# Kernel optimization log

Measured on AMD Instinct MI355X. Metric: run time of the kernel, lower is better.

Reference implementation:

```python
import jax, jax.numpy as jnp
import numpy as np

NUM_USERS = 100000
NUM_ITEMS = 50000
DIM = 64
LAYERS = 3
K = 1
N_NEGS = 16
NNZ = 2000000
BATCH = 2048
N_TOTAL = NUM_USERS + NUM_ITEMS


def setup_inputs() -> dict:
    key = jax.random.key(0)
    ks = jax.random.split(key, 8)
    return {
        "user_embed": 0.1 * jax.random.normal(ks[0], (NUM_USERS, DIM), dtype=jnp.float32),
        "item_embed": 0.1 * jax.random.normal(ks[1], (NUM_ITEMS, DIM), dtype=jnp.float32),
        "graph_vals": jax.random.uniform(ks[2], (NNZ,), dtype=jnp.float32),
        "graph_rows": jax.random.randint(ks[3], (NNZ,), 0, N_TOTAL, dtype=jnp.int32),
        "graph_cols": jax.random.randint(ks[4], (NNZ,), 0, N_TOTAL, dtype=jnp.int32),
        "user_index": jax.random.randint(ks[5], (BATCH,), 0, NUM_USERS, dtype=jnp.int32),
        "pos_index": jax.random.randint(ks[6], (BATCH,), 0, NUM_ITEMS, dtype=jnp.int32),
        "neg_index": jax.random.randint(ks[7], (BATCH, K * N_NEGS), 0, NUM_ITEMS, dtype=jnp.int32),
    }


def _spmm(vals, rows, cols, x):
    # sparse [N,N] @ dense [N,D] via gather + segment_sum
    return jax.ops.segment_sum(vals[:, None] * x[cols], rows, num_segments=N_TOTAL)


def _aggregate(user_embed, item_embed, graph_vals, graph_rows, graph_cols):
    lambdas = [(l + 1) / (LAYERS + 1) for l in range(LAYERS + 1)]
    e = jnp.concatenate([user_embed, item_embed], axis=0)  # [N, D]
    embeds = [e * lambdas[0]]
    for layer in range(LAYERS):
        e = _spmm(graph_vals, graph_rows, graph_cols, e)
        embeds.append(e * lambdas[layer + 1])
    emb = jnp.stack(embeds, axis=1)  # [N, L+1, D]
    return emb[:NUM_USERS], emb[NUM_USERS:]


def _neg_synth(user_emb, item_emb, user_index, neg_cands, pos_item, key):
    u_e = user_emb[user_index]          # [B, L+1, D]
    p_e = item_emb[pos_item]            # [B, L+1, D]
    n_e = item_emb[neg_cands]           # [B, n_negs, L+1, D]
    seed = jax.random.uniform(key, n_e.shape, dtype=n_e.dtype)
    n_e_ = seed * p_e[:, None] + (1.0 - seed) * n_e            # positive mixing
    scores = jnp.sum(u_e[:, None] * n_e_, axis=-1)             # [B, n_negs, L+1]
    idx = jnp.argmax(scores, axis=1)                            # [B, L+1]
    # select per (batch, layer) the best candidate (hop mixing)
    sel = jnp.take_along_axis(
        jnp.transpose(n_e_, (0, 2, 1, 3)),                      # [B, L+1, n_negs, D]
        idx[:, :, None, None], axis=2).squeeze(2)               # [B, L+1, D]
    return sel


def _pool(e):
    return e.reshape(e.shape[:-2] + (-1,))


def reference(user_embed, item_embed, graph_vals, graph_rows, graph_cols,
              user_index, pos_index, neg_index):
    user_emb, item_emb = _aggregate(user_embed, item_embed,
                                    graph_vals, graph_rows, graph_cols)
    nocon_u_e = user_emb[user_index]    # [B, L+1, D]
    nocon_pos_e = item_emb[pos_index]   # [B, L+1, D]
    key = jax.random.key(42)
    nocon_neg = []
    for k in range(K):
        cands = neg_index[:, k * N_NEGS:(k + 1) * N_NEGS]
        nocon_neg.append(_neg_synth(user_emb, item_emb, user_index, cands,
                                    pos_index, jax.random.fold_in(key, k)))
    nocon_neg_e = jnp.stack(nocon_neg, axis=1)  # [B, K, L+1, D]

    u_e = _pool(nocon_u_e)       # [B, (L+1)*D]
    pos_e = _pool(nocon_pos_e)
    neg_e = _pool(nocon_neg_e)   # [B, K, (L+1)*D]

    B = user_index.shape[0]
    reg_loss = 0.5 * (jnp.sum(nocon_u_e[:, 0, :] ** 2)
                      + jnp.sum(nocon_pos_e[:, 0, :] ** 2)
                      + jnp.sum(nocon_neg_e[:, :, 0, :] ** 2)) / float(B)

    pos_scores = jnp.sum(u_e * pos_e, axis=1)                 # [B]
    neg_scores = jnp.sum(u_e[:, None] * neg_e, axis=-1)       # [B, K]
    loss1 = jnp.mean(jnp.log(1.0 + jnp.sum(
        jnp.exp(neg_scores - pos_scores[:, None]), axis=1)))
    return (loss1, reg_loss)
```

## Files before the change

kernel.cpp:

```cpp
#include <hip/hip_runtime.h>

static constexpr int kNumUsers  = 100000;
static constexpr int kNumItems  = 50000;
static constexpr int kNTotal    = 150000;
static constexpr int kDim       = 64;
static constexpr int kNnz       = 2000000;
static constexpr int kBatch     = 2048;
static constexpr int kNeg       = 16;
static constexpr int kRowsPerBucket = 256;
static constexpr int kNumBuckets  = (kNTotal + kRowsPerBucket - 1) / kRowsPerBucket;
static constexpr int kBucketCap   = 4096;
static constexpr int kChunk       = 4096;
static constexpr int kEdgesPerThread = kChunk / 512;
static constexpr int kMaxList     = 2048 + 2048 + kBatch * kNeg;
static constexpr unsigned kSeedHalf = 4194304u;

typedef float f32x2 __attribute__((ext_vector_type(2)));


__device__ __forceinline__ unsigned short f2bf(float f) {
  unsigned u = __float_as_uint(f);
  unsigned r = (u + 0x7FFFu + ((u >> 16) & 1u)) >> 16;
  return (unsigned short)r;
}
__device__ __forceinline__ float bf2f(unsigned short h) {
  return __uint_as_float((unsigned)h << 16);
}


struct KeyPair { unsigned a, b; };

constexpr KeyPair tf2x32_const(unsigned k0, unsigned k1, unsigned x0, unsigned x1) {
  unsigned ks[3] = {k0, k1, k0 ^ k1 ^ 0x1BD11BDAu};
  const unsigned rots[2][4] = {{13u,15u,26u,6u},{17u,29u,16u,24u}};
  x0 += ks[0]; x1 += ks[1];
  for (int g = 0; g < 5; ++g) {
    for (int i = 0; i < 4; ++i) {
      unsigned r = rots[g & 1][i];
      x0 += x1;
      x1 = (x1 << r) | (x1 >> (32u - r));
      x1 ^= x0;
    }
    x0 += ks[(g + 1) % 3];
    x1 += ks[(g + 2) % 3] + (unsigned)(g + 1);
  }
  return {x0, x1};
}

static constexpr KeyPair kFoldedKey = tf2x32_const(0u, 42u, 0u, 0u);

__device__ __forceinline__ unsigned rotl32(unsigned x, unsigned r) {
  return (x << r) | (x >> (32u - r));
}

__device__ __forceinline__ void tf2x32(unsigned k0, unsigned k1,
                                       unsigned x0, unsigned x1,
                                       unsigned& y0, unsigned& y1) {
  const unsigned ks2 = k0 ^ k1 ^ 0x1BD11BDAu;
  x0 += k0; x1 += k1;
#define TF_ROUND(r) { x0 += x1; x1 = rotl32(x1, (r)); x1 ^= x0; }
  TF_ROUND(13u) TF_ROUND(15u) TF_ROUND(26u) TF_ROUND(6u)
  x0 += k1;  x1 += ks2 + 1u;
  TF_ROUND(17u) TF_ROUND(29u) TF_ROUND(16u) TF_ROUND(24u)
  x0 += ks2; x1 += k0 + 2u;
  TF_ROUND(13u) TF_ROUND(15u) TF_ROUND(26u) TF_ROUND(6u)
  x0 += k0;  x1 += k1 + 3u;
  TF_ROUND(17u) TF_ROUND(29u) TF_ROUND(16u) TF_ROUND(24u)
  x0 += k1;  x1 += ks2 + 4u;
  TF_ROUND(13u) TF_ROUND(15u) TF_ROUND(26u) TF_ROUND(6u)
  x0 += ks2; x1 += k0 + 5u;
#undef TF_ROUND
  y0 = x0; y1 = x1;
}

__device__ __forceinline__ float tf_uniform(unsigned i) {
  unsigned lo = (i < kSeedHalf) ? i : (i - kSeedHalf);
  unsigned hi = lo + kSeedHalf;
  unsigned y0, y1;
  tf2x32(kFoldedKey.a, kFoldedKey.b, lo, hi, y0, y1);
  unsigned bits = (i < kSeedHalf) ? y0 : y1;
  return __uint_as_float((bits >> 9) | 0x3F800000u) - 1.0f;
}

__device__ __forceinline__ float wred(float v) {
  for (int o = 32; o; o >>= 1) v += __shfl_xor(v, o, 64);
  return v;
}


__global__ void k_zero(int* __restrict__ cursor, int* __restrict__ nrows,
                       int* __restrict__ flags) {
  int i = blockIdx.x * blockDim.x + threadIdx.x;
  if (i < kNTotal) flags[i] = 0;
  if (i < kNumBuckets) cursor[i] = i * kBucketCap;
  if (i == 0) *nrows = 0;
}

__global__ void __launch_bounds__(512)
k_bscatter(const int* __restrict__ rows, const int* __restrict__ cols,
           const float* __restrict__ vals, int* __restrict__ cursor,
           int2* __restrict__ edges) {
  __shared__ int hist[kNumBuckets];
  __shared__ int base[kNumBuckets];
  int c0 = blockIdx.x * kChunk;

  int   er[kEdgesPerThread];
  int   ec[kEdgesPerThread];
  float ev[kEdgesPerThread];
  int n = 0;
#pragma unroll
  for (int i = 0; i < kEdgesPerThread; ++i) {
    int e = c0 + i * 512 + threadIdx.x;
    if (e < kNnz) {
      er[n] = rows[e];
      ec[n] = cols[e];
      ev[n] = vals[e];
      ++n;
    }
  }

  for (int i = threadIdx.x; i < kNumBuckets; i += 512) hist[i] = 0;
  __syncthreads();
  for (int i = 0; i < n; ++i) atomicAdd(&hist[er[i] >> 8], 1);
  __syncthreads();
  for (int i = threadIdx.x; i < kNumBuckets; i += 512) {
    int c = hist[i];
    base[i] = c ? atomicAdd(&cursor[i], c) : 0;
    hist[i] = 0;
  }
  __syncthreads();
  for (int i = 0; i < n; ++i) {
    int r = er[i];
    int b = r >> 8;
    int p = base[b] + atomicAdd(&hist[b], 1);
    if (p < (b + 1) * kBucketCap) {
      int2 pk;
      pk.x = ec[i] | ((r & 255) << 18);
      pk.y = __float_as_int(ev[i]);
      edges[p] = pk;
    }
  }
}

__global__ void __launch_bounds__(256)
k_bucket_csr(const int2* __restrict__ edges, const int* __restrict__ cursor,
             int2* __restrict__ edges2, int* __restrict__ rbeg, int* __restrict__ rend) {
  __shared__ int cnts[kRowsPerBucket];
  __shared__ int offs[kRowsPerBucket];
  __shared__ int wsum[4];
  int b = blockIdx.x;
  int lo = b * kBucketCap;
  int cnt = cursor[b] - lo; if (cnt > kBucketCap) cnt = kBucketCap;

  cnts[threadIdx.x] = 0;
  __syncthreads();
  for (int e = threadIdx.x; e < cnt; e += 256)
    atomicAdd(&cnts[(edges[lo + e].x >> 18) & 255], 1);
  __syncthreads();

  {
    int tid = threadIdx.x;
    int v = cnts[tid];
    int s = v;
    for (int o = 1; o < 64; o <<= 1) {
      int t = __shfl_up(s, o, 64);
      if ((tid & 63) >= o) s += t;
    }
    if ((tid & 63) == 63) wsum[tid >> 6] = s;
    __syncthreads();
    int woff = 0;
    for (int ww = 0; ww < (tid >> 6); ++ww) woff += wsum[ww];
    int excl = woff + s - v;
    offs[tid] = excl;
    int row = (b << 8) + tid;
    if (row < kNTotal) {
      rbeg[row] = lo + excl;
      rend[row] = lo + excl + v;
    }
  }
  __syncthreads();

  for (int e = threadIdx.x; e < cnt; e += 256) {
    int2 pk = edges[lo + e];
    int rl = (pk.x >> 18) & 255;
    int p = atomicAdd(&offs[rl], 1);
    edges2[lo + p] = make_int2(pk.x & 0x3FFFF, pk.y);
  }
}

__global__ void k_init_f8(const float* __restrict__ ue, const float* __restrict__ ie,
                          unsigned* __restrict__ e0f8) {
  int i = blockIdx.x * blockDim.x + threadIdx.x;
  if (i >= kNTotal * 16) return;
  const float4* __restrict__ s4 = (i < kNumUsers * 16)
    ? ((const float4*)ue + i)
    : ((const float4*)ie + (i - kNumUsers * 16));
  float4 v = *s4;
  unsigned w = 0;
  w = __builtin_amdgcn_cvt_pk_fp8_f32(v.x, v.y, w, false);
  w = __builtin_amdgcn_cvt_pk_fp8_f32(v.z, v.w, w, true);
  e0f8[i] = w;
}

__global__ void k_flag(const int* __restrict__ uidx, const int* __restrict__ pidx,
                       const int* __restrict__ nidx, int* __restrict__ flags) {
  int i = blockIdx.x * blockDim.x + threadIdx.x;
  if (i < kBatch) flags[uidx[i]] = 1;
  else if (i < 2 * kBatch) flags[kNumUsers + pidx[i - kBatch]] = 1;
  else if (i < 2 * kBatch + kBatch * kNeg) flags[kNumUsers + nidx[i - 2 * kBatch]] = 1;
}

__global__ void k_compact(const int* __restrict__ flags, int* __restrict__ rowlist,
                          int* __restrict__ nrows) {
  int i = blockIdx.x * blockDim.x + threadIdx.x;
  if (i < kNTotal && flags[i]) {
    int p = atomicAdd(nrows, 1);
    rowlist[p] = i;
  }
}

#define FMA8(d, v) {                                                      \
    f32x2 q0 = __builtin_amdgcn_cvt_pk_f32_fp8((d).x, false);             \
    f32x2 q1 = __builtin_amdgcn_cvt_pk_f32_fp8((d).x, true);              \
    f32x2 q2 = __builtin_amdgcn_cvt_pk_f32_fp8((d).y, false);             \
    f32x2 q3 = __builtin_amdgcn_cvt_pk_f32_fp8((d).y, true);              \
    a[0] += (v) * q0.x; a[1] += (v) * q0.y; a[2] += (v) * q1.x;           \
    a[3] += (v) * q1.y; a[4] += (v) * q2.x; a[5] += (v) * q2.y;           \
    a[6] += (v) * q3.x; a[7] += (v) * q3.y; }

__device__ __forceinline__ void spmm_row8(int row, int ln,
                                          const int* __restrict__ rbeg,
                                          const int* __restrict__ rend,
                                          const int2* __restrict__ edges2,
                                          const uint2* __restrict__ src8,
                                          unsigned short* __restrict__ dstbf,
                                          uint2* __restrict__ dstf8) {
  int s = rbeg[row], t = rend[row];
  float a[8];
#pragma unroll
  for (int i = 0; i < 8; ++i) a[i] = 0.0f;
  int e = s;
  for (; e + 3 < t; e += 4) {
    int2 p0 = edges2[e],     p1 = edges2[e + 1];
    int2 p2 = edges2[e + 2], p3 = edges2[e + 3];
    uint2 d0 = src8[(size_t)p0.x * 8 + ln];
    uint2 d1 = src8[(size_t)p1.x * 8 + ln];
    uint2 d2 = src8[(size_t)p2.x * 8 + ln];
    uint2 d3 = src8[(size_t)p3.x * 8 + ln];
    FMA8(d0, __int_as_float(p0.y))
    FMA8(d1, __int_as_float(p1.y))
    FMA8(d2, __int_as_float(p2.y))
    FMA8(d3, __int_as_float(p3.y))
  }
  if (e + 1 < t) {
    int2 p0 = edges2[e], p1 = edges2[e + 1];
    uint2 d0 = src8[(size_t)p0.x * 8 + ln];
    uint2 d1 = src8[(size_t)p1.x * 8 + ln];
    FMA8(d0, __int_as_float(p0.y))
    FMA8(d1, __int_as_float(p1.y))
    e += 2;
  }
  if (e < t) {
    int2 p0 = edges2[e];
    uint2 d0 = src8[(size_t)p0.x * 8 + ln];
    FMA8(d0, __int_as_float(p0.y))
  }
  uint4 ob;
  ob.x = (unsigned)f2bf(a[0]) | ((unsigned)f2bf(a[1]) << 16);
  ob.y = (unsigned)f2bf(a[2]) | ((unsigned)f2bf(a[3]) << 16);
  ob.z = (unsigned)f2bf(a[4]) | ((unsigned)f2bf(a[5]) << 16);
  ob.w = (unsigned)f2bf(a[6]) | ((unsigned)f2bf(a[7]) << 16);
  *(uint4*)(dstbf + ((size_t)row << 6) + (ln << 3)) = ob;
  if (dstf8) {
    uint2 o8;
    o8.x = 0; o8.y = 0;
    o8.x = __builtin_amdgcn_cvt_pk_fp8_f32(a[0], a[1], o8.x, false);
    o8.x = __builtin_amdgcn_cvt_pk_fp8_f32(a[2], a[3], o8.x, true);
    o8.y = __builtin_amdgcn_cvt_pk_fp8_f32(a[4], a[5], o8.y, false);
    o8.y = __builtin_amdgcn_cvt_pk_fp8_f32(a[6], a[7], o8.y, true);
    dstf8[(size_t)row * 8 + ln] = o8;
  }
}

__global__ void __launch_bounds__(256)
k_spmm_all(const int* __restrict__ rbeg, const int* __restrict__ rend,
           const int2* __restrict__ edges2, const uint2* __restrict__ src8,
           unsigned short* __restrict__ dstbf, uint2* __restrict__ dstf8) {
  int row = blockIdx.x * 32 + (threadIdx.x >> 3);
  if (row >= kNTotal) return;
  spmm_row8(row, threadIdx.x & 7, rbeg, rend, edges2, src8, dstbf, dstf8);
}

__global__ void __launch_bounds__(256)
k_spmm_list(const int* __restrict__ rbeg, const int* __restrict__ rend,
            const int2* __restrict__ edges2, const uint2* __restrict__ src8,
            unsigned short* __restrict__ dstbf, const int* __restrict__ rowlist,
            const int* __restrict__ nrows) {
  int gid = blockIdx.x * 32 + (threadIdx.x >> 3);
  if (gid >= *nrows) return;
  spmm_row8(rowlist[gid], threadIdx.x & 7, rbeg, rend, edges2, src8, dstbf, nullptr);
}

__global__ void __launch_bounds__(256)
k_batch(const float* __restrict__ ue, const float* __restrict__ ie,
        const unsigned short* __restrict__ e1, const unsigned short* __restrict__ e2,
        const unsigned short* __restrict__ e3, const int* __restrict__ uidx,
        const int* __restrict__ pidx, const int* __restrict__ nidx,
        float2* __restrict__ bout) {
  const float LAM[4] = {0.25f, 0.5f, 0.75f, 1.0f};
  int b = blockIdx.x;
  int lane = threadIdx.x & 63;
  int w = threadIdx.x >> 6;

  __shared__ float s_score[kNeg][4];
  __shared__ float s_sq0[kNeg];
  __shared__ float s_pos, s_usq, s_psq;

  int un = uidx[b];
  int pi = pidx[b];
  size_t uoff = ((size_t)un << 6) + lane;
  size_t poff = ((size_t)(kNumUsers + pi) << 6) + lane;
  float u[4], p[4];
  u[0] = ue[uoff] * LAM[0];
  p[0] = ie[((size_t)pi << 6) + lane] * LAM[0];
  u[1] = bf2f(e1[uoff]) * LAM[1]; p[1] = bf2f(e1[poff]) * LAM[1];
  u[2] = bf2f(e2[uoff]) * LAM[2]; p[2] = bf2f(e2[poff]) * LAM[2];
  u[3] = bf2f(e3[uoff]) * LAM[3]; p[3] = bf2f(e3[poff]) * LAM[3];

  if (w == 0) {
    float ps = wred(u[0]*p[0] + u[1]*p[1] + u[2]*p[2] + u[3]*p[3]);
    float uq = wred(u[0] * u[0]);
    float pq = wred(p[0] * p[0]);
    if (lane == 0) { s_pos = ps; s_usq = uq; s_psq = pq; }
  }

#pragma unroll
  for (int j = 0; j < 4; ++j) {
    int c = w * 4 + j;
    int ni = nidx[b * kNeg + c];
    size_t noff = ((size_t)(kNumUsers + ni) << 6) + lane;
#pragma unroll
    for (int l = 0; l < 4; ++l) {
      float nv;
      if (l == 0)      nv = ie[((size_t)ni << 6) + lane] * LAM[0];
      else if (l == 1) nv = bf2f(e1[noff]) * LAM[1];
      else if (l == 2) nv = bf2f(e2[noff]) * LAM[2];
      else             nv = bf2f(e3[noff]) * LAM[3];
      unsigned si = ((unsigned)(b * kNeg + c) * 4u + (unsigned)l) * 64u + (unsigned)lane;
      float sd = tf_uniform(si);
      float nm = sd * p[l] + (1.0f - sd) * nv;
      float sc = wred(u[l] * nm);
      if (l == 0) {
        float q = wred(nm * nm);
        if (lane == 0) s_sq0[c] = q;
      }
      if (lane == 0) s_score[c][l] = sc;
    }
  }
  __syncthreads();

  if (w == 0) {
    int c = lane & 15, l = lane >> 4;
    float v = s_score[c][l];
    int idx = c;
#pragma unroll
    for (int o = 1; o < 16; o <<= 1) {
      float ov = __shfl_xor(v, o, 64);
      int oi = __shfl_xor(idx, o, 64);
      bool take = (ov > v) || (ov == v && oi < idx);
      v = take ? ov : v;
      idx = take ? oi : idx;
    }
    float sum = v;
    sum += __shfl_xor(sum, 16, 64);
    sum += __shfl_xor(sum, 32, 64);
    if (lane == 0) {
      float x = sum - s_pos;
      float term = logf(1.0f + expf(x));
      float reg = 0.5f * (s_usq + s_psq + s_sq0[idx]);
      bout[b] = make_float2(term, reg);
    }
  }
}

__global__ void __launch_bounds__(256)
k_reduce(const float2* __restrict__ bout, float* __restrict__ out) {
  float t = 0.0f, r = 0.0f;
  for (int i = threadIdx.x; i < kBatch; i += 256) {
    float2 v = bout[i];
    t += v.x; r += v.y;
  }
  t = wred(t); r = wred(r);
  __shared__ float st[4], sr[4];
  int w = threadIdx.x >> 6;
  if ((threadIdx.x & 63) == 0) { st[w] = t; sr[w] = r; }
  __syncthreads();
  if (threadIdx.x == 0) {
    out[0] = (st[0] + st[1] + st[2] + st[3]) / (float)kBatch;
    out[1] = (sr[0] + sr[1] + sr[2] + sr[3]) / (float)kBatch;
  }
}


extern "C" void kernel_launch(void* const* d_in, const int* in_sizes, int n_in,
                              void* d_out, int out_size, void* d_ws, size_t ws_size,
                              hipStream_t stream) {
  const float* ue   = (const float*)d_in[0];
  const float* ie   = (const float*)d_in[1];
  const float* gv   = (const float*)d_in[2];
  const int*   gr   = (const int*)d_in[3];
  const int*   gc   = (const int*)d_in[4];
  const int*   uidx = (const int*)d_in[5];
  const int*   pidx = (const int*)d_in[6];
  const int*   nidx = (const int*)d_in[7];
  float* out = (float*)d_out;

  char* ws = (char*)d_ws;
  size_t off = 0;
  auto alloc = [&](size_t bytes) -> void* {
    off = (off + 255) & ~(size_t)255;
    void* p = ws + off;
    off += bytes;
    return p;
  };
  const size_t tblElems = (size_t)kNTotal * kDim;
  unsigned*       e0f8 = (unsigned*)      alloc(tblElems);
  unsigned short* e1bf = (unsigned short*)alloc(tblElems * 2);
  uint2*          e1f8 = (uint2*)         alloc(tblElems);
  unsigned short* e2bf = (unsigned short*)alloc(tblElems * 2);
  uint2*          e2f8 = (uint2*)         alloc(tblElems);
  unsigned short* e3bf = (unsigned short*)alloc(tblElems * 2);
  int2* edges   = (int2*)alloc((size_t)kNumBuckets * kBucketCap * sizeof(int2));
  int2* edges2  = (int2*)alloc((size_t)kNumBuckets * kBucketCap * sizeof(int2));
  int*  cursor  = (int*) alloc((size_t)kNumBuckets * sizeof(int));
  int*  rbeg    = (int*) alloc((size_t)kNTotal * sizeof(int));
  int*  rend    = (int*) alloc((size_t)kNTotal * sizeof(int));
  int*  flags   = (int*) alloc((size_t)kNTotal * sizeof(int));
  int*  rowlist = (int*) alloc((size_t)kMaxList * sizeof(int));
  int*  nrows   = (int*) alloc(16 * sizeof(int));
  float2* bout  = (float2*)alloc((size_t)kBatch * sizeof(float2));
  (void)ws_size; (void)in_sizes; (void)n_in; (void)out_size;

  hipLaunchKernelGGL(k_zero,       dim3((kNTotal + 255) / 256), dim3(256), 0, stream,
                     cursor, nrows, flags);
  hipLaunchKernelGGL(k_bscatter,   dim3((kNnz + kChunk - 1) / kChunk), dim3(512), 0, stream,
                     gr, gc, gv, cursor, edges);
  hipLaunchKernelGGL(k_init_f8,    dim3((kNTotal * 16 + 255) / 256), dim3(256), 0, stream,
                     ue, ie, e0f8);
  hipLaunchKernelGGL(k_bucket_csr, dim3(kNumBuckets),           dim3(256), 0, stream,
                     edges, cursor, edges2, rbeg, rend);
  hipLaunchKernelGGL(k_flag,       dim3((2 * kBatch + kBatch * kNeg + 255) / 256), dim3(256), 0, stream,
                     uidx, pidx, nidx, flags);
  hipLaunchKernelGGL(k_compact,    dim3((kNTotal + 255) / 256), dim3(256), 0, stream,
                     flags, rowlist, nrows);
  hipLaunchKernelGGL(k_spmm_all,   dim3((kNTotal + 31) / 32),   dim3(256), 0, stream,
                     rbeg, rend, edges2, (const uint2*)e0f8, e1bf, e1f8);
  hipLaunchKernelGGL(k_spmm_all,   dim3((kNTotal + 31) / 32),   dim3(256), 0, stream,
                     rbeg, rend, edges2, e1f8, e2bf, e2f8);
  hipLaunchKernelGGL(k_spmm_list,  dim3((kMaxList + 31) / 32),  dim3(256), 0, stream,
                     rbeg, rend, edges2, e2f8, e3bf, rowlist, nrows);
  hipLaunchKernelGGL(k_batch,      dim3(kBatch),                dim3(256), 0, stream,
                     ue, ie, e1bf, e2bf, e3bf, uidx, pidx, nidx, bout);
  hipLaunchKernelGGL(k_reduce,     dim3(1),                     dim3(256), 0, stream, bout, out);
}
```

Baseline: 197.7 us.

## Fuse setup kernels, pad bucket cursors, share Threefry output across batch pairs

Merges the zero-fill and fp8 conversion kernels into one launch, and replaces the flag plus full-range compaction pass with an atomicExch-based dedup that builds the row list directly. Bucket cursors are padded to a stride of 16 ints so that global atomics on different buckets stop contending on the same cache line. The batch kernel now handles samples b and b+B/2 in one block, using both outputs of a single Threefry call for their paired random indices, which halves the RNG work and the number of blocks. The trade-off is more register pressure in the batch kernel, and the row list order now depends on atomic timing.

```diff
diff --git a/kernel.cpp b/kernel.cpp
--- a/kernel.cpp
+++ b/kernel.cpp
@@ -12,6 +12,7 @@
 static constexpr int kBucketCap   = 4096;
 static constexpr int kChunk       = 4096;
 static constexpr int kEdgesPerThread = kChunk / 512;
+static constexpr int kCurStride   = 16;
 static constexpr int kMaxList     = 2048 + 2048 + kBatch * kNeg;
 static constexpr unsigned kSeedHalf = 4194304u;
 
@@ -73,12 +74,7 @@
   y0 = x0; y1 = x1;
 }
 
-__device__ __forceinline__ float tf_uniform(unsigned i) {
-  unsigned lo = (i < kSeedHalf) ? i : (i - kSeedHalf);
-  unsigned hi = lo + kSeedHalf;
-  unsigned y0, y1;
-  tf2x32(kFoldedKey.a, kFoldedKey.b, lo, hi, y0, y1);
-  unsigned bits = (i < kSeedHalf) ? y0 : y1;
+__device__ __forceinline__ float bits2f(unsigned bits) {
   return __uint_as_float((bits >> 9) | 0x3F800000u) - 1.0f;
 }
 
@@ -88,11 +84,22 @@
 }
 
 
-__global__ void k_zero(int* __restrict__ cursor, int* __restrict__ nrows,
-                       int* __restrict__ flags) {
+__global__ void k_zeroinit(const float* __restrict__ ue, const float* __restrict__ ie,
+                           unsigned* __restrict__ e0f8, int* __restrict__ cursor,
+                           int* __restrict__ nrows, int* __restrict__ flags) {
   int i = blockIdx.x * blockDim.x + threadIdx.x;
+  if (i < kNTotal * 16) {
+    const float4* __restrict__ s4 = (i < kNumUsers * 16)
+      ? ((const float4*)ue + i)
+      : ((const float4*)ie + (i - kNumUsers * 16));
+    float4 v = *s4;
+    unsigned w = 0;
+    w = __builtin_amdgcn_cvt_pk_fp8_f32(v.x, v.y, w, false);
+    w = __builtin_amdgcn_cvt_pk_fp8_f32(v.z, v.w, w, true);
+    e0f8[i] = w;
+  }
   if (i < kNTotal) flags[i] = 0;
-  if (i < kNumBuckets) cursor[i] = i * kBucketCap;
+  if (i < kNumBuckets) cursor[i * kCurStride] = i * kBucketCap;
   if (i == 0) *nrows = 0;
 }
 
@@ -125,7 +132,7 @@
   __syncthreads();
   for (int i = threadIdx.x; i < kNumBuckets; i += 512) {
     int c = hist[i];
-    base[i] = c ? atomicAdd(&cursor[i], c) : 0;
+    base[i] = c ? atomicAdd(&cursor[i * kCurStride], c) : 0;
     hist[i] = 0;
   }
   __syncthreads();
@@ -150,7 +157,7 @@
   __shared__ int wsum[4];
   int b = blockIdx.x;
   int lo = b * kBucketCap;
-  int cnt = cursor[b] - lo; if (cnt > kBucketCap) cnt = kBucketCap;
+  int cnt = cursor[b * kCurStride] - lo; if (cnt > kBucketCap) cnt = kBucketCap;
 
   cnts[threadIdx.x] = 0;
   __syncthreads();
@@ -188,34 +195,17 @@
   }
 }
 
-__global__ void k_init_f8(const float* __restrict__ ue, const float* __restrict__ ie,
-                          unsigned* __restrict__ e0f8) {
+__global__ void k_flaglist(const int* __restrict__ uidx, const int* __restrict__ pidx,
+                           const int* __restrict__ nidx, int* __restrict__ flags,
+                           int* __restrict__ rowlist, int* __restrict__ nrows) {
   int i = blockIdx.x * blockDim.x + threadIdx.x;
-  if (i >= kNTotal * 16) return;
-  const float4* __restrict__ s4 = (i < kNumUsers * 16)
-    ? ((const float4*)ue + i)
-    : ((const float4*)ie + (i - kNumUsers * 16));
-  float4 v = *s4;
-  unsigned w = 0;
-  w = __builtin_amdgcn_cvt_pk_fp8_f32(v.x, v.y, w, false);
-  w = __builtin_amdgcn_cvt_pk_fp8_f32(v.z, v.w, w, true);
-  e0f8[i] = w;
-}
-
-__global__ void k_flag(const int* __restrict__ uidx, const int* __restrict__ pidx,
-                       const int* __restrict__ nidx, int* __restrict__ flags) {
-  int i = blockIdx.x * blockDim.x + threadIdx.x;
-  if (i < kBatch) flags[uidx[i]] = 1;
-  else if (i < 2 * kBatch) flags[kNumUsers + pidx[i - kBatch]] = 1;
-  else if (i < 2 * kBatch + kBatch * kNeg) flags[kNumUsers + nidx[i - 2 * kBatch]] = 1;
-}
-
-__global__ void k_compact(const int* __restrict__ flags, int* __restrict__ rowlist,
-                          int* __restrict__ nrows) {
-  int i = blockIdx.x * blockDim.x + threadIdx.x;
-  if (i < kNTotal && flags[i]) {
+  int node = -1;
+  if (i < kBatch) node = uidx[i];
+  else if (i < 2 * kBatch) node = kNumUsers + pidx[i - kBatch];
+  else if (i < 2 * kBatch + kBatch * kNeg) node = kNumUsers + nidx[i - 2 * kBatch];
+  if (node >= 0 && atomicExch(&flags[node], 1) == 0) {
     int p = atomicAdd(nrows, 1);
-    rowlist[p] = i;
+    rowlist[p] = node;
   }
 }
 
@@ -308,60 +298,79 @@
         const int* __restrict__ pidx, const int* __restrict__ nidx,
         float2* __restrict__ bout) {
   const float LAM[4] = {0.25f, 0.5f, 0.75f, 1.0f};
-  int b = blockIdx.x;
+  int b0 = blockIdx.x;
+  int b1 = b0 + kBatch / 2;
   int lane = threadIdx.x & 63;
   int w = threadIdx.x >> 6;
 
-  __shared__ float s_score[kNeg][4];
-  __shared__ float s_sq0[kNeg];
-  __shared__ float s_pos, s_usq, s_psq;
-
-  int un = uidx[b];
-  int pi = pidx[b];
-  size_t uoff = ((size_t)un << 6) + lane;
-  size_t poff = ((size_t)(kNumUsers + pi) << 6) + lane;
-  float u[4], p[4];
-  u[0] = ue[uoff] * LAM[0];
-  p[0] = ie[((size_t)pi << 6) + lane] * LAM[0];
-  u[1] = bf2f(e1[uoff]) * LAM[1]; p[1] = bf2f(e1[poff]) * LAM[1];
-  u[2] = bf2f(e2[uoff]) * LAM[2]; p[2] = bf2f(e2[poff]) * LAM[2];
-  u[3] = bf2f(e3[uoff]) * LAM[3]; p[3] = bf2f(e3[poff]) * LAM[3];
+  __shared__ float s_score[2][kNeg][4];
+  __shared__ float s_sq0[2][kNeg];
+  __shared__ float s_pos[2], s_usq[2], s_psq[2];
+
+  int un0 = uidx[b0], pi0 = pidx[b0];
+  int un1 = uidx[b1], pi1 = pidx[b1];
+  size_t uo0 = ((size_t)un0 << 6) + lane, po0 = ((size_t)(kNumUsers + pi0) << 6) + lane;
+  size_t uo1 = ((size_t)un1 << 6) + lane, po1 = ((size_t)(kNumUsers + pi1) << 6) + lane;
+  float u0[4], p0[4], u1[4], p1[4];
+  u0[0] = ue[uo0] * LAM[0]; p0[0] = ie[((size_t)pi0 << 6) + lane] * LAM[0];
+  u1[0] = ue[uo1] * LAM[0]; p1[0] = ie[((size_t)pi1 << 6) + lane] * LAM[0];
+  u0[1] = bf2f(e1[uo0]) * LAM[1]; p0[1] = bf2f(e1[po0]) * LAM[1];
+  u1[1] = bf2f(e1[uo1]) * LAM[1]; p1[1] = bf2f(e1[po1]) * LAM[1];
+  u0[2] = bf2f(e2[uo0]) * LAM[2]; p0[2] = bf2f(e2[po0]) * LAM[2];
+  u1[2] = bf2f(e2[uo1]) * LAM[2]; p1[2] = bf2f(e2[po1]) * LAM[2];
+  u0[3] = bf2f(e3[uo0]) * LAM[3]; p0[3] = bf2f(e3[po0]) * LAM[3];
+  u1[3] = bf2f(e3[uo1]) * LAM[3]; p1[3] = bf2f(e3[po1]) * LAM[3];
 
   if (w == 0) {
-    float ps = wred(u[0]*p[0] + u[1]*p[1] + u[2]*p[2] + u[3]*p[3]);
-    float uq = wred(u[0] * u[0]);
-    float pq = wred(p[0] * p[0]);
-    if (lane == 0) { s_pos = ps; s_usq = uq; s_psq = pq; }
+    float ps = wred(u0[0]*p0[0] + u0[1]*p0[1] + u0[2]*p0[2] + u0[3]*p0[3]);
+    float uq = wred(u0[0] * u0[0]);
+    float pq = wred(p0[0] * p0[0]);
+    if (lane == 0) { s_pos[0] = ps; s_usq[0] = uq; s_psq[0] = pq; }
+  } else if (w == 1) {
+    float ps = wred(u1[0]*p1[0] + u1[1]*p1[1] + u1[2]*p1[2] + u1[3]*p1[3]);
+    float uq = wred(u1[0] * u1[0]);
+    float pq = wred(p1[0] * p1[0]);
+    if (lane == 0) { s_pos[1] = ps; s_usq[1] = uq; s_psq[1] = pq; }
   }
 
 #pragma unroll
   for (int j = 0; j < 4; ++j) {
     int c = w * 4 + j;
-    int ni = nidx[b * kNeg + c];
-    size_t noff = ((size_t)(kNumUsers + ni) << 6) + lane;
+    int ni0 = nidx[b0 * kNeg + c];
+    int ni1 = nidx[b1 * kNeg + c];
+    size_t no0 = ((size_t)(kNumUsers + ni0) << 6) + lane;
+    size_t no1 = ((size_t)(kNumUsers + ni1) << 6) + lane;
 #pragma unroll
     for (int l = 0; l < 4; ++l) {
-      float nv;
-      if (l == 0)      nv = ie[((size_t)ni << 6) + lane] * LAM[0];
-      else if (l == 1) nv = bf2f(e1[noff]) * LAM[1];
-      else if (l == 2) nv = bf2f(e2[noff]) * LAM[2];
-      else             nv = bf2f(e3[noff]) * LAM[3];
-      unsigned si = ((unsigned)(b * kNeg + c) * 4u + (unsigned)l) * 64u + (unsigned)lane;
-      float sd = tf_uniform(si);
-      float nm = sd * p[l] + (1.0f - sd) * nv;
-      float sc = wred(u[l] * nm);
+      float nv0, nv1;
       if (l == 0) {
-        float q = wred(nm * nm);
-        if (lane == 0) s_sq0[c] = q;
+        nv0 = ie[((size_t)ni0 << 6) + lane] * LAM[0];
+        nv1 = ie[((size_t)ni1 << 6) + lane] * LAM[0];
+      } else if (l == 1) { nv0 = bf2f(e1[no0]) * LAM[1]; nv1 = bf2f(e1[no1]) * LAM[1]; }
+      else if (l == 2)   { nv0 = bf2f(e2[no0]) * LAM[2]; nv1 = bf2f(e2[no1]) * LAM[2]; }
+      else               { nv0 = bf2f(e3[no0]) * LAM[3]; nv1 = bf2f(e3[no1]) * LAM[3]; }
+      unsigned si = ((unsigned)(b0 * kNeg + c) * 4u + (unsigned)l) * 64u + (unsigned)lane;
+      unsigned y0, y1;
+      tf2x32(kFoldedKey.a, kFoldedKey.b, si, si + kSeedHalf, y0, y1);
+      float sd0 = bits2f(y0);
+      float sd1 = bits2f(y1);
+      float nm0 = sd0 * p0[l] + (1.0f - sd0) * nv0;
+      float nm1 = sd1 * p1[l] + (1.0f - sd1) * nv1;
+      float sc0 = wred(u0[l] * nm0);
+      float sc1 = wred(u1[l] * nm1);
+      if (l == 0) {
+        float q0 = wred(nm0 * nm0);
+        float q1 = wred(nm1 * nm1);
+        if (lane == 0) { s_sq0[0][c] = q0; s_sq0[1][c] = q1; }
       }
-      if (lane == 0) s_score[c][l] = sc;
-    }
-  }
-  __syncthreads();
-
-  if (w == 0) {
+      if (lane == 0) { s_score[0][c][l] = sc0; s_score[1][c][l] = sc1; }
+    }
+  }
+  __syncthreads();
+
+  if (w < 2) {
     int c = lane & 15, l = lane >> 4;
-    float v = s_score[c][l];
+    float v = s_score[w][c][l];
     int idx = c;
 #pragma unroll
     for (int o = 1; o < 16; o <<= 1) {
@@ -375,10 +384,10 @@
     sum += __shfl_xor(sum, 16, 64);
     sum += __shfl_xor(sum, 32, 64);
     if (lane == 0) {
-      float x = sum - s_pos;
+      float x = sum - s_pos[w];
       float term = logf(1.0f + expf(x));
-      float reg = 0.5f * (s_usq + s_psq + s_sq0[idx]);
-      bout[b] = make_float2(term, reg);
+      float reg = 0.5f * (s_usq[w] + s_psq[w] + s_sq0[w][idx]);
+      bout[w == 0 ? b0 : b1] = make_float2(term, reg);
     }
   }
 }
@@ -432,7 +441,7 @@
   unsigned short* e3bf = (unsigned short*)alloc(tblElems * 2);
   int2* edges   = (int2*)alloc((size_t)kNumBuckets * kBucketCap * sizeof(int2));
   int2* edges2  = (int2*)alloc((size_t)kNumBuckets * kBucketCap * sizeof(int2));
-  int*  cursor  = (int*) alloc((size_t)kNumBuckets * sizeof(int));
+  int*  cursor  = (int*) alloc((size_t)kNumBuckets * kCurStride * sizeof(int));
   int*  rbeg    = (int*) alloc((size_t)kNTotal * sizeof(int));
   int*  rend    = (int*) alloc((size_t)kNTotal * sizeof(int));
   int*  flags   = (int*) alloc((size_t)kNTotal * sizeof(int));
@@ -441,25 +450,21 @@
   float2* bout  = (float2*)alloc((size_t)kBatch * sizeof(float2));
   (void)ws_size; (void)in_sizes; (void)n_in; (void)out_size;
 
-  hipLaunchKernelGGL(k_zero,       dim3((kNTotal + 255) / 256), dim3(256), 0, stream,
-                     cursor, nrows, flags);
+  hipLaunchKernelGGL(k_zeroinit,   dim3((kNTotal * 16 + 255) / 256), dim3(256), 0, stream,
+                     ue, ie, e0f8, cursor, nrows, flags);
   hipLaunchKernelGGL(k_bscatter,   dim3((kNnz + kChunk - 1) / kChunk), dim3(512), 0, stream,
                      gr, gc, gv, cursor, edges);
-  hipLaunchKernelGGL(k_init_f8,    dim3((kNTotal * 16 + 255) / 256), dim3(256), 0, stream,
-                     ue, ie, e0f8);
   hipLaunchKernelGGL(k_bucket_csr, dim3(kNumBuckets),           dim3(256), 0, stream,
                      edges, cursor, edges2, rbeg, rend);
-  hipLaunchKernelGGL(k_flag,       dim3((2 * kBatch + kBatch * kNeg + 255) / 256), dim3(256), 0, stream,
-                     uidx, pidx, nidx, flags);
-  hipLaunchKernelGGL(k_compact,    dim3((kNTotal + 255) / 256), dim3(256), 0, stream,
-                     flags, rowlist, nrows);
+  hipLaunchKernelGGL(k_flaglist,   dim3((2 * kBatch + kBatch * kNeg + 255) / 256), dim3(256), 0, stream,
+                     uidx, pidx, nidx, flags, rowlist, nrows);
   hipLaunchKernelGGL(k_spmm_all,   dim3((kNTotal + 31) / 32),   dim3(256), 0, stream,
                      rbeg, rend, edges2, (const uint2*)e0f8, e1bf, e1f8);
   hipLaunchKernelGGL(k_spmm_all,   dim3((kNTotal + 31) / 32),   dim3(256), 0, stream,
                      rbeg, rend, edges2, e1f8, e2bf, e2f8);
   hipLaunchKernelGGL(k_spmm_list,  dim3((kMaxList + 31) / 32),  dim3(256), 0, stream,
                      rbeg, rend, edges2, e2f8, e3bf, rowlist, nrows);
-  hipLaunchKernelGGL(k_batch,      dim3(kBatch),                dim3(256), 0, stream,
+  hipLaunchKernelGGL(k_batch,      dim3(kBatch / 2),            dim3(256), 0, stream,
                      ue, ie, e1bf, e2bf, e3bf, uidx, pidx, nidx, bout);
   hipLaunchKernelGGL(k_reduce,     dim3(1),                     dim3(256), 0, stream, bout, out);
 }
```

Result: faster. 178.1 us (-9.9%).
